# Kernel optimization log

Measured on AMD Instinct MI355X. Metric: run time of the kernel, lower is better.

The kernel has to match this reference:

```python
import jax, jax.numpy as jnp
import numpy as np

N_BINS = 15


def setup_inputs() -> dict:
    key = jax.random.key(0)
    k1, k2 = jax.random.split(key)
    logits = jax.random.normal(k1, (4, 19, 512, 1024), dtype=jnp.float32)
    labels = jax.random.randint(k2, (4, 512, 1024), 0, 19)
    return {"logits": logits, "labels": labels}


def reference(logits, labels):
    # logits: [B, C, H, W], labels: [B, H, W]
    C = logits.shape[1]
    conf = jax.nn.softmax(logits, axis=1)                     # [B, C, H, W]
    conf = jnp.moveaxis(conf, 1, 0).reshape(C, -1)            # [C, N], N = B*H*W
    N = conf.shape[1]

    lab = labels.reshape(-1)                                  # [N]
    lab_eq = (lab[None, :] == jnp.arange(C)[:, None]).astype(jnp.float32)  # [C, N]

    # Bin i covers (i/n_bins, (i+1)/n_bins]; conf == 0 falls in no bin
    # (matches torch's gt(lower) * le(upper) with boundaries linspace(0,1)).
    bin_idx = jnp.clip(jnp.ceil(conf * N_BINS).astype(jnp.int32) - 1, 0, N_BINS - 1)
    valid = conf > 0.0
    seg = jnp.where(valid, jnp.arange(C, dtype=jnp.int32)[:, None] * N_BINS + bin_idx,
                    C * N_BINS).reshape(-1)                   # dump segment for invalid
    num_seg = C * N_BINS + 1

    ones = jnp.ones((C * N,), dtype=jnp.float32)
    counts = jax.ops.segment_sum(ones, seg, num_segments=num_seg)[: C * N_BINS].reshape(C, N_BINS)
    acc_sum = jax.ops.segment_sum(lab_eq.reshape(-1), seg, num_segments=num_seg)[: C * N_BINS].reshape(C, N_BINS)
    conf_sum = jax.ops.segment_sum(conf.reshape(-1), seg, num_segments=num_seg)[: C * N_BINS].reshape(C, N_BINS)

    nonzero = counts > 0
    safe = jnp.where(nonzero, counts, 1.0)
    avg_conf = conf_sum / safe
    acc = acc_sum / safe
    # prop_in_bin = counts / N (mean over the full class plane)
    per_class = jnp.sum(jnp.where(nonzero, jnp.abs(avg_conf - acc) * counts / N, 0.0), axis=1)  # [C]
    sce = jnp.mean(per_class)
    return sce
```

## Files before the change

kernel.cpp:

```cpp
#include <hip/hip_runtime.h>
#include <stdint.h>

#define C_    19
#define NB    15
#define CB    (C_ * NB)
#define HW    (512 * 1024)
#define NPIX  (4 * HW)
#define TPB   256
#define TILE  256
#define ROWS  20
#define NT    8
#define GBLK  (NPIX / (TILE * NT))
#define REPS  8
#define KCOP  8

__global__ __launch_bounds__(TPB, 3)
void ece_hist(const float* __restrict__ logits,
              const int*   __restrict__ labels,
              float*       __restrict__ ws) {
    __shared__ uint32_t tile[2][ROWS][TILE];
    __shared__ float    hist[REPS * CB];

    const int tid  = threadIdx.x;
    const int wave = tid >> 6;
    const int lane = tid & 63;

    for (int i = tid; i < REPS * CB; i += TPB) hist[i] = 0.f;
    __syncthreads();

    float* myh = hist + (tid & (REPS - 1)) * CB;

    float d0[C_], d1[C_];
#pragma unroll
    for (int c = 0; c < C_; ++c) { d0[c] = 0.f; d1[c] = 0.f; }

    auto STAGE = [&](int t, int bb) {
        const int n0 = (blockIdx.x * NT + t) * TILE;
        const int b  = n0 >> 19;
        const int hw = n0 & (HW - 1);
#pragma unroll
        for (int k = 0; k < 5; ++k) {
            const int r = wave * 5 + k;
            const uint32_t* src = (r < C_)
                ? (const uint32_t*)(logits + ((size_t)b * C_ + r) * HW + hw) + lane * 4
                : (const uint32_t*)(labels + n0) + lane * 4;
            __builtin_amdgcn_global_load_lds(
                (const __attribute__((address_space(1))) void*)src,
                (__attribute__((address_space(3))) void*)&tile[bb][r][0],
                16, 0, 0);
        }
    };

    STAGE(0, 0);
    for (int t = 0; t < NT; ++t) {
        const int cur = t & 1;
        if (t + 1 < NT) {
            STAGE(t + 1, cur ^ 1);
            asm volatile("s_waitcnt vmcnt(5)" ::: "memory");
        } else {
            asm volatile("s_waitcnt vmcnt(0)" ::: "memory");
        }
        __builtin_amdgcn_s_barrier();
        __builtin_amdgcn_sched_barrier(0);

        float x[C_];
#pragma unroll
        for (int c = 0; c < C_; ++c) x[c] = __uint_as_float(tile[cur][c][tid]);
        const int l = (int)tile[cur][C_][tid];

        float s = 0.f;
#pragma unroll
        for (int c = 0; c < C_; ++c) { x[c] = __expf(x[c]); s += x[c]; }
        const float inv = 1.f / s;

#pragma unroll
        for (int c = 0; c < C_; ++c) {
            const float conf = x[c] * inv;
            int bin = (int)ceilf(conf * (float)NB) - 1;
            bin = bin < 0 ? 0 : (bin > NB - 1 ? NB - 1 : bin);
            const float val = conf - ((c == l) ? 1.f : 0.f);
            d0[c] += (bin == 0) ? val : 0.f;
            d1[c] += (bin == 1) ? val : 0.f;
            if (bin >= 2) atomicAdd(&myh[c * NB + bin], val);
        }

        __builtin_amdgcn_s_barrier();
    }

#pragma unroll
    for (int c = 0; c < C_; ++c) {
        float v0 = d0[c], v1 = d1[c];
        v0 += __shfl_xor(v0, 1); v1 += __shfl_xor(v1, 1);
        v0 += __shfl_xor(v0, 2); v1 += __shfl_xor(v1, 2);
        v0 += __shfl_xor(v0, 4); v1 += __shfl_xor(v1, 4);
        if ((tid & 7) == 0) {
            const int r = (tid >> 3) & (REPS - 1);
            atomicAdd(&hist[r * CB + c * NB + 0], v0);
            atomicAdd(&hist[r * CB + c * NB + 1], v1);
        }
    }
    __syncthreads();

    float* wsb = ws + (size_t)(blockIdx.x & (KCOP - 1)) * CB;
    for (int i = tid; i < CB; i += TPB) {
        float s = 0.f;
#pragma unroll
        for (int r = 0; r < REPS; ++r) s += hist[r * CB + i];
        atomicAdd(&wsb[i], s);
    }
}

__global__ void ece_final(const float* __restrict__ ws, float* __restrict__ out) {
    const int t = threadIdx.x;
    float val = 0.f;
    if (t < CB) {
        float s = 0.f;
#pragma unroll
        for (int k = 0; k < KCOP; ++k) s += ws[k * CB + t];
        val = fabsf(s);
    }
#pragma unroll
    for (int off = 32; off; off >>= 1) val += __shfl_down(val, off);
    __shared__ float sm[5];
    if ((t & 63) == 0) sm[t >> 6] = val;
    __syncthreads();
    if (t == 0) {
        float tot = sm[0] + sm[1] + sm[2] + sm[3] + sm[4];
        out[0] = tot / ((float)NPIX * (float)C_);
    }
}

extern "C" void kernel_launch(void* const* d_in, const int* in_sizes, int n_in,
                              void* d_out, int out_size, void* d_ws, size_t ws_size,
                              hipStream_t stream) {
    const float* logits = (const float*)d_in[0];
    const int*   labels = (const int*)d_in[1];
    float* out = (float*)d_out;
    float* ws  = (float*)d_ws;

    hipMemsetAsync(ws, 0, (size_t)KCOP * CB * sizeof(float), stream);
    ece_hist<<<GBLK, TPB, 0, stream>>>(logits, labels, ws);
    ece_final<<<1, 320, 0, stream>>>(ws, out);
}
```

Baseline: 58.27 us.

## Give each wave a private LDS tile to drop block-wide barriers

Each wave now stages its own 64-pixel tiles into a private LDS region with 4-byte global_load_lds copies, so the two per-iteration block barriers are removed and waves run independently. The softmax denominator is summed as a tree to shorten the dependency chain, and the shared histogram replica count drops from 8 to 4. The cost is 20 small 4-byte async loads per stage instead of 5 16-byte loads, which raises instruction and memory-request count. It also risks more LDS atomic contention per replica.

```diff
diff --git a/kernel.cpp b/kernel.cpp
--- a/kernel.cpp
+++ b/kernel.cpp
@@ -7,18 +7,18 @@
 #define HW    (512 * 1024)
 #define NPIX  (4 * HW)
 #define TPB   256
-#define TILE  256
+#define WTILE 64
 #define ROWS  20
 #define NT    8
-#define GBLK  (NPIX / (TILE * NT))
-#define REPS  8
+#define GBLK  (NPIX / (WTILE * NT * 4))
+#define REPS  4
 #define KCOP  8
 
 __global__ __launch_bounds__(TPB, 3)
 void ece_hist(const float* __restrict__ logits,
               const int*   __restrict__ labels,
               float*       __restrict__ ws) {
-    __shared__ uint32_t tile[2][ROWS][TILE];
+    __shared__ uint32_t tile[4][2][ROWS][WTILE];
     __shared__ float    hist[REPS * CB];
 
     const int tid  = threadIdx.x;
@@ -35,19 +35,18 @@
     for (int c = 0; c < C_; ++c) { d0[c] = 0.f; d1[c] = 0.f; }
 
     auto STAGE = [&](int t, int bb) {
-        const int n0 = (blockIdx.x * NT + t) * TILE;
+        const int n0 = ((blockIdx.x * 4 + wave) * NT + t) * WTILE;
         const int b  = n0 >> 19;
         const int hw = n0 & (HW - 1);
 #pragma unroll
-        for (int k = 0; k < 5; ++k) {
-            const int r = wave * 5 + k;
+        for (int r = 0; r < ROWS; ++r) {
             const uint32_t* src = (r < C_)
-                ? (const uint32_t*)(logits + ((size_t)b * C_ + r) * HW + hw) + lane * 4
-                : (const uint32_t*)(labels + n0) + lane * 4;
+                ? (const uint32_t*)(logits + ((size_t)b * C_ + r) * HW + hw) + lane
+                : (const uint32_t*)(labels + n0) + lane;
             __builtin_amdgcn_global_load_lds(
                 (const __attribute__((address_space(1))) void*)src,
-                (__attribute__((address_space(3))) void*)&tile[bb][r][0],
-                16, 0, 0);
+                (__attribute__((address_space(3))) void*)&tile[wave][bb][r][0],
+                4, 0, 0);
         }
     };
 
@@ -56,22 +55,27 @@
         const int cur = t & 1;
         if (t + 1 < NT) {
             STAGE(t + 1, cur ^ 1);
-            asm volatile("s_waitcnt vmcnt(5)" ::: "memory");
+            asm volatile("s_waitcnt vmcnt(20)" ::: "memory");
         } else {
             asm volatile("s_waitcnt vmcnt(0)" ::: "memory");
         }
-        __builtin_amdgcn_s_barrier();
         __builtin_amdgcn_sched_barrier(0);
 
         float x[C_];
 #pragma unroll
-        for (int c = 0; c < C_; ++c) x[c] = __uint_as_float(tile[cur][c][tid]);
-        const int l = (int)tile[cur][C_][tid];
+        for (int c = 0; c < C_; ++c) x[c] = __uint_as_float(tile[wave][cur][c][lane]);
+        const int l = (int)tile[wave][cur][C_][lane];
 
-        float s = 0.f;
 #pragma unroll
-        for (int c = 0; c < C_; ++c) { x[c] = __expf(x[c]); s += x[c]; }
-        const float inv = 1.f / s;
+        for (int c = 0; c < C_; ++c) x[c] = __expf(x[c]);
+
+        float a[10];
+#pragma unroll
+        for (int j = 0; j < 9; ++j) a[j] = x[2 * j] + x[2 * j + 1];
+        a[9] = x[18];
+        a[0] += a[1]; a[2] += a[3]; a[4] += a[5]; a[6] += a[7]; a[8] += a[9];
+        a[0] += a[2]; a[4] += a[6];
+        const float inv = 1.f / (a[0] + a[4] + a[8]);
 
 #pragma unroll
         for (int c = 0; c < C_; ++c) {
@@ -83,8 +87,6 @@
             d1[c] += (bin == 1) ? val : 0.f;
             if (bin >= 2) atomicAdd(&myh[c * NB + bin], val);
         }
-
-        __builtin_amdgcn_s_barrier();
     }
 
 #pragma unroll
```

After: 57.61 us. No clear change (-1.1%).
